# Kernel tuning notes

Hardware: AMD Instinct MI355X
Metric: run time of the kernel (lower is better)

Reference implementation:

```python
import jax, jax.numpy as jnp
import numpy as np

VOCAB, H, E_DIM, N_HEADS, MAXSEQ, L, N_ROUTED, TOPK = 32000, 1024, 512, 16, 1024, 4, 10, 3
EPS = 1e-5


def layernorm(x, g, b):
    m = jnp.mean(x, axis=-1, keepdims=True)
    v = jnp.mean((x - m) ** 2, axis=-1, keepdims=True)
    return (x - m) / jnp.sqrt(v + EPS) * g + b


def causal_attn(x, Wqkv, Wo):
    B, T, C = x.shape
    Dh = C // N_HEADS
    qkv = x @ Wqkv                                    # [B,T,3C]
    q, k, v = jnp.split(qkv, 3, axis=-1)
    def heads(t):  # [B,T,C] -> [B,Hh,T,Dh]
        return t.reshape(B, T, N_HEADS, Dh).transpose(0, 2, 1, 3)
    q, k, v = heads(q), heads(k), heads(v)
    scores = jnp.einsum('bhqd,bhkd->bhqk', q, k) / jnp.sqrt(jnp.float32(Dh))
    mask = jnp.tril(jnp.ones((T, T), dtype=bool))
    scores = jnp.where(mask, scores, jnp.finfo(scores.dtype).min)
    att = jax.nn.softmax(scores, axis=-1)
    y = jnp.einsum('bhqk,bhkd->bhqd', att, v)
    y = y.transpose(0, 2, 1, 3).reshape(B, T, C)
    return y @ Wo


def moe(x, Wr, Wsu, Wsd, Wu, Wd):
    # shared expert (n_shared=1)
    shared = jax.nn.gelu(x @ Wsu, approximate=False) @ Wsd
    # router + top-k gates
    probs = jax.nn.softmax(x @ Wr, axis=-1)           # [B,T,E]
    vals, idx = jax.lax.top_k(probs, TOPK)            # [B,T,k]
    gates = jnp.einsum('btke,btk->bte', jax.nn.one_hot(idx, N_ROUTED, dtype=x.dtype), vals)
    # routed experts: dense-over-experts compute, gate-weighted combine
    up = jax.nn.gelu(jnp.einsum('btd,edf->ebtf', x, Wu), approximate=False)
    out = jnp.einsum('ebtf,efd->ebtd', up, Wd)
    routed = jnp.einsum('ebtd,bte->btd', out, gates)
    return shared + routed


def forward(x, W_emb, W_pos, ln1_g, ln1_b, Wqkv, Wo, ln2_g, ln2_b,
            Wr, Wsu, Wsd, Wu, Wd, lnf_g, lnf_b):
    B, T = x.shape
    h = W_emb[x] + W_pos[:T][None, :, :]
    for l in range(L):
        a = causal_attn(layernorm(h, ln1_g[l], ln1_b[l]), Wqkv[l], Wo[l])
        a = a + h                                     # attn residual
        m = moe(layernorm(a, ln2_g[l], ln2_b[l]), Wr[l], Wsu[l], Wsd[l], Wu[l], Wd[l])
        h = m + h                                     # NOTE: residual from block INPUT (as in source)
    h = layernorm(h, lnf_g, lnf_b)
    logits = h[:, -1:, :] @ W_emb.T                   # tied head, last position only
    return logits


def setup_inputs() -> dict:
    key = jax.random.key(0)
    ks = jax.random.split(key, 16)
    s = 0.02
    d = {
        'x': jax.random.randint(ks[0], (4, 1024), 0, VOCAB),
        'W_emb': s * jax.random.normal(ks[1], (VOCAB, H), jnp.float32),
        'W_pos': s * jax.random.normal(ks[2], (MAXSEQ, H), jnp.float32),
        'ln1_g': jnp.ones((L, H), jnp.float32),
        'ln1_b': jnp.zeros((L, H), jnp.float32),
        'Wqkv': s * jax.random.normal(ks[3], (L, H, 3 * H), jnp.float32),
        'Wo': s * jax.random.normal(ks[4], (L, H, H), jnp.float32),
        'ln2_g': jnp.ones((L, H), jnp.float32),
        'ln2_b': jnp.zeros((L, H), jnp.float32),
        'Wr': s * jax.random.normal(ks[5], (L, H, N_ROUTED), jnp.float32),
        'Wsu': s * jax.random.normal(ks[6], (L, H, E_DIM), jnp.float32),
        'Wsd': s * jax.random.normal(ks[7], (L, E_DIM, H), jnp.float32),
        'Wu': s * jax.random.normal(ks[8], (L, N_ROUTED, H, E_DIM), jnp.float32),
        'Wd': s * jax.random.normal(ks[9], (L, N_ROUTED, E_DIM, H), jnp.float32),
        'lnf_g': jnp.ones((H,), jnp.float32),
        'lnf_b': jnp.zeros((H,), jnp.float32),
    }
    return d


def reference(x, W_emb, W_pos, ln1_g, ln1_b, Wqkv, Wo, ln2_g, ln2_b,
              Wr, Wsu, Wsd, Wu, Wd, lnf_g, lnf_b):
    return forward(x, W_emb, W_pos, ln1_g, ln1_b, Wqkv, Wo, ln2_g, ln2_b,
                   Wr, Wsu, Wsd, Wu, Wd, lnf_g, lnf_b)
```

## Files before the change

### kernel.cpp

```cpp
#include <hip/hip_runtime.h>
#include <hip/hip_bf16.h>
#include <math.h>

#define BT 4096
#define HD 1024
#define NHEAD 16
#define DH 64
#define ED 512
#define NEXP 10
#define NEXPA 11
#define TOPKE 3
#define NLAYER 4
#define NVOCAB 32000
#define NSLOT (BT * TOPKE)
#define NSLOTA (NSLOT + BT)
#define NSB 12

typedef __attribute__((ext_vector_type(8))) short bf16x8;
typedef __attribute__((ext_vector_type(4))) short bf16x4;
typedef __attribute__((ext_vector_type(4))) float f32x4;

__device__ __forceinline__ float gelu_f(float x) {
  return 0.5f * x * (1.0f + erff(x * 0.70710678118654752440f));
}

__device__ __forceinline__ void gll16(const void* g, void* l) {
  __builtin_amdgcn_global_load_lds(
      (const __attribute__((address_space(1))) unsigned int*)g,
      (__attribute__((address_space(3))) unsigned int*)l, 16, 0, 0);
}

__global__ __launch_bounds__(256) void k_embed_ln(const int* __restrict__ x,
                                                  const float* __restrict__ Wemb,
                                                  const float* __restrict__ Wpos,
                                                  const float* __restrict__ g,
                                                  const float* __restrict__ b,
                                                  float* __restrict__ h,
                                                  __hip_bfloat16* __restrict__ outb) {
  const int t = blockIdx.x;
  const int tid = threadIdx.x;
  const int pos = t & 1023;
  const int tok = x[t];
  float4 a = ((const float4*)(Wemb + (size_t)tok * HD))[tid];
  float4 p = ((const float4*)(Wpos + (size_t)pos * HD))[tid];
  float4 v = make_float4(a.x + p.x, a.y + p.y, a.z + p.z, a.w + p.w);
  ((float4*)(h + (size_t)t * HD))[tid] = v;
  float s = v.x + v.y + v.z + v.w;
  float ss = v.x * v.x + v.y * v.y + v.z * v.z + v.w * v.w;
#pragma unroll
  for (int o = 32; o > 0; o >>= 1) { s += __shfl_down(s, o); ss += __shfl_down(ss, o); }
  __shared__ float rs[4], rss[4];
  if ((tid & 63) == 0) { rs[tid >> 6] = s; rss[tid >> 6] = ss; }
  __syncthreads();
  const float S = rs[0] + rs[1] + rs[2] + rs[3];
  const float SS = rss[0] + rss[1] + rss[2] + rss[3];
  const float mean = S * (1.0f / HD);
  const float inv = rsqrtf(SS * (1.0f / HD) - mean * mean + 1e-5f);
  const float4 gg = ((const float4*)g)[tid];
  const float4 bb = ((const float4*)b)[tid];
  union { bf16x4 v; __hip_bfloat16 e[4]; } u;
  u.e[0] = __float2bfloat16((v.x - mean) * inv * gg.x + bb.x);
  u.e[1] = __float2bfloat16((v.y - mean) * inv * gg.y + bb.y);
  u.e[2] = __float2bfloat16((v.z - mean) * inv * gg.z + bb.z);
  u.e[3] = __float2bfloat16((v.w - mean) * inv * gg.w + bb.w);
  *(bf16x4*)(outb + (size_t)t * HD + tid * 4) = u.v;
}

__global__ __launch_bounds__(256) void k_wtrans(const float* __restrict__ in,
                                                __hip_bfloat16* __restrict__ out,
                                                int K, int N,
                                                int srcPer, int dstPer, int dstOff) {
  const int z = blockIdx.z;
  const int dz = (z / srcPer) * dstPer + (z % srcPer) + dstOff;
  const float* src = in + (size_t)z * K * N;
  __hip_bfloat16* dst = out + (size_t)dz * N * K;
  __shared__ float t[64][65];
  const int tid = threadIdx.x;
  const int k0 = blockIdx.y * 64, n0 = blockIdx.x * 64;
#pragma unroll
  for (int i = 0; i < 4; ++i) {
    const int r = (tid >> 4) + i * 16;
    const int c = (tid & 15) * 4;
    float4 v = *(const float4*)(src + (size_t)(k0 + r) * N + n0 + c);
    t[r][c] = v.x; t[r][c + 1] = v.y; t[r][c + 2] = v.z; t[r][c + 3] = v.w;
  }
  __syncthreads();
#pragma unroll
  for (int i = 0; i < 2; ++i) {
    const int n = (tid >> 3) + i * 32;
    const int k = (tid & 7) * 8;
    union { bf16x8 v; __hip_bfloat16 e[8]; } u;
#pragma unroll
    for (int j = 0; j < 8; ++j) u.e[j] = __float2bfloat16(t[k + j][n]);
    *(bf16x8*)(dst + (size_t)(n0 + n) * K + k0 + k) = u.v;
  }
}

__global__ __launch_bounds__(256) void k_wrtrans(const float* __restrict__ in,
                                                 float* __restrict__ out) {
  const int l = blockIdx.x;
  const float* src = in + (size_t)l * HD * NEXP;
  float* dst = out + (size_t)l * NEXP * HD;
  for (int idx = threadIdx.x; idx < NEXP * HD; idx += 256) {
    const int e = idx / HD, k = idx - e * HD;
    dst[idx] = src[(size_t)k * NEXP + e];
  }
}

__global__ __launch_bounds__(256) void k_vtrans(const __hip_bfloat16* __restrict__ qkv,
                                                __hip_bfloat16* __restrict__ vt) {
  const int bh = blockIdx.x, tt = blockIdx.y;
  const int b = bh >> 4, h = bh & 15;
  __shared__ __hip_bfloat16 t[64][72];
  for (int c = threadIdx.x; c < 512; c += 256) {
    int r = c >> 3, d0 = (c & 7) * 8;
    *(bf16x8*)&t[r][d0] =
        *(const bf16x8*)(qkv + ((size_t)(b * 1024 + tt * 64 + r)) * 3072 + 2048 + h * 64 + d0);
  }
  __syncthreads();
  for (int c = threadIdx.x; c < 512; c += 256) {
    int d = c >> 3, t0 = (c & 7) * 8;
    union { bf16x8 v; __hip_bfloat16 e[8]; } u;
#pragma unroll
    for (int j = 0; j < 8; ++j) u.e[j] = t[t0 + j][d];
    *(bf16x8*)(vt + ((size_t)(bh * 64 + d)) * 1024 + tt * 64 + t0) = u.v;
  }
}

__global__ __launch_bounds__(256) void k_ln_router(const __hip_bfloat16* __restrict__ in,
                                                   const float* __restrict__ g,
                                                   const float* __restrict__ b,
                                                   const float* __restrict__ Wrt,
                                                   __hip_bfloat16* __restrict__ outb,
                                                   float* __restrict__ gates,
                                                   int* __restrict__ eidx) {
  const int row = blockIdx.x;
  const int tid = threadIdx.x;
  __shared__ float xs[HD];
  __shared__ float rs[4], rss[4];
  __shared__ float lg[16];
  union { bf16x4 v; __hip_bfloat16 e[4]; } iv;
  iv.v = *(const bf16x4*)(in + (size_t)row * HD + tid * 4);
  const float4 v = make_float4(__bfloat162float(iv.e[0]), __bfloat162float(iv.e[1]),
                               __bfloat162float(iv.e[2]), __bfloat162float(iv.e[3]));
  float s = v.x + v.y + v.z + v.w;
  float ss = v.x * v.x + v.y * v.y + v.z * v.z + v.w * v.w;
#pragma unroll
  for (int o = 32; o > 0; o >>= 1) { s += __shfl_down(s, o); ss += __shfl_down(ss, o); }
  if ((tid & 63) == 0) { rs[tid >> 6] = s; rss[tid >> 6] = ss; }
  __syncthreads();
  const float S = rs[0] + rs[1] + rs[2] + rs[3];
  const float SS = rss[0] + rss[1] + rss[2] + rss[3];
  const float mean = S * (1.0f / HD);
  const float inv = rsqrtf(SS * (1.0f / HD) - mean * mean + 1e-5f);
  const float4 gg = ((const float4*)g)[tid];
  const float4 bb = ((const float4*)b)[tid];
  const float o0 = (v.x - mean) * inv * gg.x + bb.x;
  const float o1 = (v.y - mean) * inv * gg.y + bb.y;
  const float o2 = (v.z - mean) * inv * gg.z + bb.z;
  const float o3 = (v.w - mean) * inv * gg.w + bb.w;
  union { bf16x4 v; __hip_bfloat16 e[4]; } u;
  u.e[0] = __float2bfloat16(o0); u.e[1] = __float2bfloat16(o1);
  u.e[2] = __float2bfloat16(o2); u.e[3] = __float2bfloat16(o3);
  *(bf16x4*)(outb + (size_t)row * HD + tid * 4) = u.v;
  ((float4*)xs)[tid] = make_float4(o0, o1, o2, o3);
  __syncthreads();
  const int wv = tid >> 6, lane = tid & 63;
  for (int e = wv; e < NEXP; e += 4) {
    const float4* wr4 = (const float4*)(Wrt + (size_t)e * HD);
    float d = 0.f;
#pragma unroll
    for (int i = 0; i < 4; ++i) {
      float4 xv = ((const float4*)xs)[lane + i * 64];
      float4 wv4 = wr4[lane + i * 64];
      d += xv.x * wv4.x + xv.y * wv4.y + xv.z * wv4.z + xv.w * wv4.w;
    }
#pragma unroll
    for (int o = 32; o > 0; o >>= 1) d += __shfl_down(d, o);
    if (lane == 0) lg[e] = d;
  }
  __syncthreads();
  if (tid == 0) {
    float m = lg[0];
#pragma unroll
    for (int e = 1; e < NEXP; ++e) m = fmaxf(m, lg[e]);
    float p[NEXP], sum = 0.f;
#pragma unroll
    for (int e = 0; e < NEXP; ++e) { p[e] = __expf(lg[e] - m); sum += p[e]; }
    const float isum = 1.0f / sum;
#pragma unroll
    for (int e = 0; e < NEXP; ++e) p[e] *= isum;
    bool used[NEXP] = {};
    for (int k = 0; k < TOPKE; ++k) {
      int best = -1; float bv = -1.f;
      for (int e = 0; e < NEXP; ++e)
        if (!used[e] && p[e] > bv) { bv = p[e]; best = e; }
      used[best] = true;
      eidx[row * TOPKE + k] = best;
      gates[row * TOPKE + k] = bv;
    }
  }
}

__global__ __launch_bounds__(256) void k_lnf(const float* __restrict__ h,
                                             const float* __restrict__ g,
                                             const float* __restrict__ b,
                                             float* __restrict__ hf) {
  const int row = blockIdx.x * 1024 + 1023;
  const int tid = threadIdx.x;
  const float* xr = h + (size_t)row * HD;
  float s = 0.f, ss = 0.f;
  for (int i = tid; i < HD; i += 256) { float v = xr[i]; s += v; ss += v * v; }
#pragma unroll
  for (int o = 32; o > 0; o >>= 1) { s += __shfl_down(s, o); ss += __shfl_down(ss, o); }
  __shared__ float rs[4], rss[4];
  if ((tid & 63) == 0) { rs[tid >> 6] = s; rss[tid >> 6] = ss; }
  __syncthreads();
  const float S = rs[0] + rs[1] + rs[2] + rs[3];
  const float SS = rss[0] + rss[1] + rss[2] + rss[3];
  const float mean = S * (1.0f / HD);
  const float inv = rsqrtf(SS * (1.0f / HD) - mean * mean + 1e-5f);
  float* orow = hf + (size_t)blockIdx.x * HD;
  for (int i = tid; i < HD; i += 256) {
    float v = xr[i];
    orow[i] = (v - mean) * inv * g[i] + b[i];
  }
}

template <int EPI, int OBF>
__global__ __launch_bounds__(256) void k_mgemm(const __hip_bfloat16* __restrict__ A,
                                               const __hip_bfloat16* __restrict__ Bt,
                                               const float* __restrict__ R,
                                               float* __restrict__ C,
                                               __hip_bfloat16* __restrict__ Cb,
                                               int M, int N, int K) {
  __shared__ __hip_bfloat16 As[128 * 32];
  __shared__ __hip_bfloat16 Bs[128 * 32];
  const int tid = threadIdx.x;
  const int w = tid >> 6, lane = tid & 63;
  const int wr = w >> 1, wc = w & 1;
  const int m0 = blockIdx.y << 7, n0 = blockIdx.x << 7;
  const int srow = lane >> 2;
  const int scol = (lane & 3) * 8;
  const int kq = (lane >> 4) * 8;
  int aidx[4], bidx[4];
#pragma unroll
  for (int m = 0; m < 4; ++m) aidx[m] = (wr * 64 + m * 16 + (lane & 15)) * 32 + kq;
#pragma unroll
  for (int n = 0; n < 4; ++n) bidx[n] = (wc * 64 + n * 16 + (lane & 15)) * 32 + kq;

  f32x4 acc[4][4];
#pragma unroll
  for (int m = 0; m < 4; ++m)
#pragma unroll
    for (int n = 0; n < 4; ++n) acc[m][n] = (f32x4){0.f, 0.f, 0.f, 0.f};

  const __hip_bfloat16* ga = A + (size_t)(m0 + w * 32 + srow) * K + scol;
  const __hip_bfloat16* gb = Bt + (size_t)(n0 + w * 32 + srow) * K + scol;
  __hip_bfloat16* la0 = &As[(w * 32) * 32];
  __hip_bfloat16* la1 = &As[(w * 32 + 16) * 32];
  __hip_bfloat16* lb0 = &Bs[(w * 32) * 32];
  __hip_bfloat16* lb1 = &Bs[(w * 32 + 16) * 32];

  for (int k0 = 0; k0 < K; k0 += 32) {
    gll16(ga + k0, la0);
    gll16(ga + (size_t)16 * K + k0, la1);
    gll16(gb + k0, lb0);
    gll16(gb + (size_t)16 * K + k0, lb1);
    __syncthreads();
    bf16x8 af[4], bfv[4];
#pragma unroll
    for (int m = 0; m < 4; ++m) af[m] = *(const bf16x8*)&As[aidx[m]];
#pragma unroll
    for (int n = 0; n < 4; ++n) bfv[n] = *(const bf16x8*)&Bs[bidx[n]];
#pragma unroll
    for (int m = 0; m < 4; ++m)
#pragma unroll
      for (int n = 0; n < 4; ++n)
        acc[m][n] = __builtin_amdgcn_mfma_f32_16x16x32_bf16(af[m], bfv[n], acc[m][n], 0, 0, 0);
    __syncthreads();
  }

#pragma unroll
  for (int m = 0; m < 4; ++m) {
#pragma unroll
    for (int n = 0; n < 4; ++n) {
#pragma unroll
      for (int r = 0; r < 4; ++r) {
        const int row = m0 + wr * 64 + m * 16 + (lane >> 4) * 4 + r;
        const int col = n0 + wc * 64 + n * 16 + (lane & 15);
        float v = acc[m][n][r];
        if (EPI == 2) v += R[(size_t)row * N + col];
        if (OBF) Cb[(size_t)row * N + col] = __float2bfloat16(v);
        else C[(size_t)row * N + col] = v;
      }
    }
  }
}

template <int EPI>
__global__ __launch_bounds__(256) void k_mgemm_moe(const __hip_bfloat16* __restrict__ A,
                                                   const __hip_bfloat16* __restrict__ Btbase,
                                                   __hip_bfloat16* __restrict__ Cb,
                                                   const int* __restrict__ counts,
                                                   const int* __restrict__ offs,
                                                   const int* __restrict__ row_slot,
                                                   const float* __restrict__ gate_slot,
                                                   int N, int K, int gather) {
  int T = blockIdx.y;
  int e = -1, r0 = 0, acc0 = 0;
#pragma unroll
  for (int ee = 0; ee < NEXPA; ++ee) {
    const int nt = (counts[ee] + 127) >> 7;
    if (e < 0 && T < acc0 + nt) { e = ee; r0 = (T - acc0) << 7; }
    acc0 += nt;
  }
  if (e < 0) return;
  const int cnt = counts[e], off = offs[e];
  const __hip_bfloat16* Bt = Btbase + (size_t)e * N * K;

  __shared__ __hip_bfloat16 As[128 * 32];
  __shared__ __hip_bfloat16 Bs[128 * 32];
  const int tid = threadIdx.x;
  const int w = tid >> 6, lane = tid & 63;
  const int wr = w >> 1, wc = w & 1;
  const int n0 = blockIdx.x << 7;
  const int srow = lane >> 2;
  const int scol = (lane & 3) * 8;
  const int kq = (lane >> 4) * 8;
  int aidx[4], bidx[4];
#pragma unroll
  for (int m = 0; m < 4; ++m) aidx[m] = (wr * 64 + m * 16 + (lane & 15)) * 32 + kq;
#pragma unroll
  for (int n = 0; n < 4; ++n) bidx[n] = (wc * 64 + n * 16 + (lane & 15)) * 32 + kq;

  const int last = off + cnt - 1;
  int s0 = off + r0 + w * 32 + srow;        if (s0 > last) s0 = last;
  int s1 = off + r0 + w * 32 + 16 + srow;   if (s1 > last) s1 = last;
  const int arow0 = gather ? row_slot[s0] : s0;
  const int arow1 = gather ? row_slot[s1] : s1;

  f32x4 acc[4][4];
#pragma unroll
  for (int m = 0; m < 4; ++m)
#pragma unroll
    for (int n = 0; n < 4; ++n) acc[m][n] = (f32x4){0.f, 0.f, 0.f, 0.f};

  const __hip_bfloat16* ga0 = A + (size_t)arow0 * K + scol;
  const __hip_bfloat16* ga1 = A + (size_t)arow1 * K + scol;
  const __hip_bfloat16* gb = Bt + (size_t)(n0 + w * 32 + srow) * K + scol;
  __hip_bfloat16* la0 = &As[(w * 32) * 32];
  __hip_bfloat16* la1 = &As[(w * 32 + 16) * 32];
  __hip_bfloat16* lb0 = &Bs[(w * 32) * 32];
  __hip_bfloat16* lb1 = &Bs[(w * 32 + 16) * 32];

  for (int k0 = 0; k0 < K; k0 += 32) {
    gll16(ga0 + k0, la0);
    gll16(ga1 + k0, la1);
    gll16(gb + k0, lb0);
    gll16(gb + (size_t)16 * K + k0, lb1);
    __syncthreads();
    bf16x8 af[4], bfv[4];
#pragma unroll
    for (int m = 0; m < 4; ++m) af[m] = *(const bf16x8*)&As[aidx[m]];
#pragma unroll
    for (int n = 0; n < 4; ++n) bfv[n] = *(const bf16x8*)&Bs[bidx[n]];
#pragma unroll
    for (int m = 0; m < 4; ++m)
#pragma unroll
      for (int n = 0; n < 4; ++n)
        acc[m][n] = __builtin_amdgcn_mfma_f32_16x16x32_bf16(af[m], bfv[n], acc[m][n], 0, 0, 0);
    __syncthreads();
  }

#pragma unroll
  for (int m = 0; m < 4; ++m) {
#pragma unroll
    for (int r = 0; r < 4; ++r) {
      const int rl = wr * 64 + m * 16 + (lane >> 4) * 4 + r;
      if (r0 + rl < cnt) {
        const int slot = off + r0 + rl;
        const float sc = (EPI == 3) ? gate_slot[slot] : 1.0f;
#pragma unroll
        for (int n = 0; n < 4; ++n) {
          const int col = n0 + wc * 64 + n * 16 + (lane & 15);
          float v = acc[m][n][r];
          if (EPI == 1) v = gelu_f(v);
          else v *= sc;
          Cb[(size_t)slot * N + col] = __float2bfloat16(v);
        }
      }
    }
  }
}

__global__ __launch_bounds__(256) void k_mattn(const __hip_bfloat16* __restrict__ qkv,
                                               const __hip_bfloat16* __restrict__ vt,
                                               __hip_bfloat16* __restrict__ y) {
  const int bh = blockIdx.x;
  const int qt = 7 - (int)blockIdx.y;
  const int b = bh >> 4, hh = bh & 15;
  const int tid = threadIdx.x;
  const int w = tid >> 6, lane = tid & 63;
  const int l15 = lane & 15, g = lane >> 4;
  const int swl = (l15 & 7) << 3;

  __shared__ __hip_bfloat16 Ks[64 * 64];
  __shared__ __hip_bfloat16 Vs[64 * 64];
  __shared__ __hip_bfloat16 Pw[2][4][16 * 64];

  bf16x8 qf[2][2];
#pragma unroll
  for (int s = 0; s < 2; ++s) {
    const __hip_bfloat16* qp =
        qkv + ((size_t)(b * 1024 + qt * 128 + s * 64 + w * 16 + l15)) * 3072 + hh * 64 + g * 8;
    qf[s][0] = *(const bf16x8*)qp;
    qf[s][1] = *(const bf16x8*)(qp + 32);
  }

  f32x4 yacc[2][4];
#pragma unroll
  for (int s = 0; s < 2; ++s)
#pragma unroll
    for (int nt = 0; nt < 4; ++nt) yacc[s][nt] = (f32x4){0.f, 0.f, 0.f, 0.f};
  float m_s[2] = {-INFINITY, -INFINITY};
  float l_s[2] = {0.f, 0.f};
  const int qg0 = qt * 128 + w * 16 + l15;

  const int ktmax = 2 * qt + 1;
  for (int kt = 0; kt <= ktmax; ++kt) {
    __syncthreads();
#pragma unroll
    for (int c0 = 0; c0 < 512; c0 += 256) {
      const int c = c0 + tid;
      const int r = c >> 3, cc = (c & 7) * 8;
      const int sw = cc ^ ((r & 7) << 3);
      *(bf16x8*)&Ks[r * 64 + sw] =
          *(const bf16x8*)(qkv + ((size_t)(b * 1024 + kt * 64 + r)) * 3072 + 1024 + hh * 64 + cc);
      *(bf16x8*)&Vs[r * 64 + sw] =
          *(const bf16x8*)(vt + ((size_t)(bh * 64 + r)) * 1024 + kt * 64 + cc);
    }
    __syncthreads();
    bf16x8 kf[4][2];
#pragma unroll
    for (int m = 0; m < 4; ++m) {
      const int row = m * 16 + l15;
#pragma unroll
      for (int kk = 0; kk < 2; ++kk)
        kf[m][kk] = *(const bf16x8*)&Ks[row * 64 + ((kk * 32 + g * 8) ^ swl)];
    }
    bf16x8 pa[2][2] = {};
#pragma unroll
    for (int s = 0; s < 2; ++s) {
      if (kt > 2 * qt + s) continue;
      f32x4 st[4];
#pragma unroll
      for (int m = 0; m < 4; ++m) st[m] = (f32x4){0.f, 0.f, 0.f, 0.f};
#pragma unroll
      for (int m = 0; m < 4; ++m)
#pragma unroll
        for (int kk = 0; kk < 2; ++kk)
          st[m] = __builtin_amdgcn_mfma_f32_16x16x32_bf16(kf[m][kk], qf[s][kk], st[m], 0, 0, 0);
      const int qg = qg0 + s * 64;
      const bool dia = (kt == 2 * qt + s);
      float tmax = -INFINITY;
#pragma unroll
      for (int m = 0; m < 4; ++m)
#pragma unroll
        for (int r = 0; r < 4; ++r) {
          float v = st[m][r] * 0.125f;
          if (dia && (kt * 64 + m * 16 + g * 4 + r) > qg) v = -INFINITY;
          st[m][r] = v;
          tmax = fmaxf(tmax, v);
        }
      tmax = fmaxf(tmax, __shfl_xor(tmax, 16));
      tmax = fmaxf(tmax, __shfl_xor(tmax, 32));
      const float mnew = fmaxf(m_s[s], tmax);
      const float fac = __expf(m_s[s] - mnew);
      m_s[s] = mnew;
      float tsum = 0.f;
#pragma unroll
      for (int m = 0; m < 4; ++m)
#pragma unroll
        for (int r = 0; r < 4; ++r) {
          float p = __expf(st[m][r] - mnew);
          st[m][r] = p;
          tsum += p;
        }
      tsum += __shfl_xor(tsum, 16);
      tsum += __shfl_xor(tsum, 32);
      l_s[s] = l_s[s] * fac + tsum;
      float fq[4];
#pragma unroll
      for (int r = 0; r < 4; ++r) fq[r] = __shfl(fac, g * 4 + r);
#pragma unroll
      for (int nt = 0; nt < 4; ++nt)
#pragma unroll
        for (int r = 0; r < 4; ++r) yacc[s][nt][r] *= fq[r];
#pragma unroll
      for (int m = 0; m < 4; ++m) {
        union { bf16x4 v; __hip_bfloat16 e[4]; } pk;
#pragma unroll
        for (int r = 0; r < 4; ++r) pk.e[r] = __float2bfloat16(st[m][r]);
        *(bf16x4*)&Pw[s][w][l15 * 64 + ((m * 16 + g * 4) ^ swl)] = pk.v;
      }
#pragma unroll
      for (int kk = 0; kk < 2; ++kk)
        pa[s][kk] = *(const bf16x8*)&Pw[s][w][l15 * 64 + ((kk * 32 + g * 8) ^ swl)];
    }
    const bool v0 = (kt <= 2 * qt);
#pragma unroll
    for (int kk = 0; kk < 2; ++kk)
#pragma unroll
      for (int nt = 0; nt < 4; ++nt) {
        bf16x8 vf = *(const bf16x8*)&Vs[(nt * 16 + l15) * 64 + ((kk * 32 + g * 8) ^ swl)];
        if (v0) yacc[0][nt] = __builtin_amdgcn_mfma_f32_16x16x32_bf16(pa[0][kk], vf, yacc[0][nt], 0, 0, 0);
        yacc[1][nt] = __builtin_amdgcn_mfma_f32_16x16x32_bf16(pa[1][kk], vf, yacc[1][nt], 0, 0, 0);
      }
  }
#pragma unroll
  for (int s = 0; s < 2; ++s) {
    const float inv = 1.0f / l_s[s];
    float iq[4];
#pragma unroll
    for (int r = 0; r < 4; ++r) iq[r] = __shfl(inv, g * 4 + r);
#pragma unroll
    for (int r = 0; r < 4; ++r) {
      __hip_bfloat16* yp =
          y + ((size_t)(b * 1024 + qt * 128 + s * 64 + w * 16 + g * 4 + r)) * HD + hh * 64 + l15;
#pragma unroll
      for (int nt = 0; nt < 4; ++nt)
        yp[nt * 16] = __float2bfloat16(yacc[s][nt][r] * iq[r]);
    }
  }
}

__global__ __launch_bounds__(1024) void k_hist(const int* __restrict__ eidx,
                                               int* __restrict__ hist_g) {
  __shared__ int lh[16];
  const int tid = threadIdx.x;
  if (tid < 16) lh[tid] = 0;
  __syncthreads();
  atomicAdd(&lh[eidx[blockIdx.x * 1024 + tid]], 1);
  __syncthreads();
  if (tid < 16) hist_g[blockIdx.x * 16 + tid] = lh[tid];
}

__global__ __launch_bounds__(1024) void k_scatter2(const int* __restrict__ eidx,
                                                   const float* __restrict__ gates,
                                                   const int* __restrict__ hist_g,
                                                   int* __restrict__ counts,
                                                   int* __restrict__ offs,
                                                   int* __restrict__ row_slot,
                                                   float* __restrict__ gate_slot,
                                                   int* __restrict__ slot_of) {
  __shared__ int lcur[16];
  const int tid = threadIdx.x;
  const int blk = blockIdx.x;
  if (tid == 0) {
    int off = 0;
    for (int e = 0; e < NEXP; ++e) {
      int pre = 0, tot = 0;
      for (int b = 0; b < NSB; ++b) {
        const int hc = hist_g[b * 16 + e];
        if (b < blk) pre += hc;
        tot += hc;
      }
      lcur[e] = off + pre;
      if (blk == 0) { counts[e] = tot; offs[e] = off; }
      off += tot;
    }
    if (blk == 0) { counts[NEXP] = BT; offs[NEXP] = NSLOT; }
  }
  __syncthreads();
  const int i = blk * 1024 + tid;
  const int e = eidx[i];
  const int pos = atomicAdd(&lcur[e], 1);
  row_slot[pos] = i / TOPKE;
  gate_slot[pos] = gates[i];
  slot_of[i] = pos;
  if (i < BT) { row_slot[NSLOT + i] = i; gate_slot[NSLOT + i] = 1.0f; }
}

template <int DOLN>
__global__ __launch_bounds__(256) void k_combine_ln(float* __restrict__ h,
                                                    const __hip_bfloat16* __restrict__ rd,
                                                    const int* __restrict__ slot_of,
                                                    const float* __restrict__ g,
                                                    const float* __restrict__ b,
                                                    __hip_bfloat16* __restrict__ outb) {
  const int t = blockIdx.x;
  const int tid = threadIdx.x;
  const int s0 = slot_of[t * 3 + 0], s1 = slot_of[t * 3 + 1], s2 = slot_of[t * 3 + 2];
  const int s3 = NSLOT + t;
  float4 hv = ((float4*)(h + (size_t)t * HD))[tid];
  union { bf16x4 v; __hip_bfloat16 e[4]; } r0, r1, r2, r3;
  r0.v = *(const bf16x4*)(rd + (size_t)s0 * HD + tid * 4);
  r1.v = *(const bf16x4*)(rd + (size_t)s1 * HD + tid * 4);
  r2.v = *(const bf16x4*)(rd + (size_t)s2 * HD + tid * 4);
  r3.v = *(const bf16x4*)(rd + (size_t)s3 * HD + tid * 4);
  hv.x += __bfloat162float(r0.e[0]) + __bfloat162float(r1.e[0]) + __bfloat162float(r2.e[0]) + __bfloat162float(r3.e[0]);
  hv.y += __bfloat162float(r0.e[1]) + __bfloat162float(r1.e[1]) + __bfloat162float(r2.e[1]) + __bfloat162float(r3.e[1]);
  hv.z += __bfloat162float(r0.e[2]) + __bfloat162float(r1.e[2]) + __bfloat162float(r2.e[2]) + __bfloat162float(r3.e[2]);
  hv.w += __bfloat162float(r0.e[3]) + __bfloat162float(r1.e[3]) + __bfloat162float(r2.e[3]) + __bfloat162float(r3.e[3]);
  ((float4*)(h + (size_t)t * HD))[tid] = hv;
  if (DOLN) {
    float s = hv.x + hv.y + hv.z + hv.w;
    float ss = hv.x * hv.x + hv.y * hv.y + hv.z * hv.z + hv.w * hv.w;
#pragma unroll
    for (int o = 32; o > 0; o >>= 1) { s += __shfl_down(s, o); ss += __shfl_down(ss, o); }
    __shared__ float rs[4], rss[4];
    if ((tid & 63) == 0) { rs[tid >> 6] = s; rss[tid >> 6] = ss; }
    __syncthreads();
    const float S = rs[0] + rs[1] + rs[2] + rs[3];
    const float SS = rss[0] + rss[1] + rss[2] + rss[3];
    const float mean = S * (1.0f / HD);
    const float inv = rsqrtf(SS * (1.0f / HD) - mean * mean + 1e-5f);
    const float4 gg = ((const float4*)g)[tid];
    const float4 bb = ((const float4*)b)[tid];
    union { bf16x4 v; __hip_bfloat16 e[4]; } u;
    u.e[0] = __float2bfloat16((hv.x - mean) * inv * gg.x + bb.x);
    u.e[1] = __float2bfloat16((hv.y - mean) * inv * gg.y + bb.y);
    u.e[2] = __float2bfloat16((hv.z - mean) * inv * gg.z + bb.z);
    u.e[3] = __float2bfloat16((hv.w - mean) * inv * gg.w + bb.w);
    *(bf16x4*)(outb + (size_t)t * HD + tid * 4) = u.v;
  }
}

__global__ __launch_bounds__(256) void k_head(const float* __restrict__ hf,
                                              const float* __restrict__ Wemb,
                                              float* __restrict__ out) {
  __shared__ float hs[4][HD];
  const int tid = threadIdx.x;
  for (int i = tid; i < HD; i += 256) {
    hs[0][i] = hf[i]; hs[1][i] = hf[HD + i];
    hs[2][i] = hf[2 * HD + i]; hs[3][i] = hf[3 * HD + i];
  }
  __syncthreads();
  const int w = tid >> 6, lane = tid & 63;
  for (int i = 0; i < 4; ++i) {
    const int v = blockIdx.x * 16 + w * 4 + i;
    const float4* wr = (const float4*)(Wemb + (size_t)v * HD);
    float a0 = 0.f, a1 = 0.f, a2 = 0.f, a3 = 0.f;
    for (int q = lane; q < HD / 4; q += 64) {
      float4 wv = wr[q];
      const int k = q * 4;
      a0 += wv.x * hs[0][k] + wv.y * hs[0][k + 1] + wv.z * hs[0][k + 2] + wv.w * hs[0][k + 3];
      a1 += wv.x * hs[1][k] + wv.y * hs[1][k + 1] + wv.z * hs[1][k + 2] + wv.w * hs[1][k + 3];
      a2 += wv.x * hs[2][k] + wv.y * hs[2][k + 1] + wv.z * hs[2][k + 2] + wv.w * hs[2][k + 3];
      a3 += wv.x * hs[3][k] + wv.y * hs[3][k + 1] + wv.z * hs[3][k + 2] + wv.w * hs[3][k + 3];
    }
#pragma unroll
    for (int o = 32; o > 0; o >>= 1) {
      a0 += __shfl_down(a0, o); a1 += __shfl_down(a1, o);
      a2 += __shfl_down(a2, o); a3 += __shfl_down(a3, o);
    }
    if (lane == 0) {
      out[v] = a0; out[NVOCAB + v] = a1;
      out[2 * NVOCAB + v] = a2; out[3 * NVOCAB + v] = a3;
    }
  }
}

extern "C" void kernel_launch(void* const* d_in, const int* in_sizes, int n_in,
                              void* d_out, int out_size, void* d_ws, size_t ws_size,
                              hipStream_t stream) {
  (void)in_sizes; (void)n_in; (void)out_size; (void)ws_size;
  const int* x = (const int*)d_in[0];
  const float* W_emb = (const float*)d_in[1];
  const float* W_pos = (const float*)d_in[2];
  const float* ln1_g = (const float*)d_in[3];
  const float* ln1_b = (const float*)d_in[4];
  const float* Wqkv = (const float*)d_in[5];
  const float* Wo = (const float*)d_in[6];
  const float* ln2_g = (const float*)d_in[7];
  const float* ln2_b = (const float*)d_in[8];
  const float* Wr = (const float*)d_in[9];
  const float* Wsu = (const float*)d_in[10];
  const float* Wsd = (const float*)d_in[11];
  const float* Wu = (const float*)d_in[12];
  const float* Wd = (const float*)d_in[13];
  const float* lnf_g = (const float*)d_in[14];
  const float* lnf_b = (const float*)d_in[15];
  float* out = (float*)d_out;

  float* wsf = (float*)d_ws;
  size_t o = 0;
  float* hbuf = wsf + o; o += (size_t)BT * HD;
  float* hf = wsf + o; o += 4 * HD;
  float* gates = wsf + o; o += NSLOT;
  float* gate_slot = wsf + o; o += NSLOTA;
  int* eidx = (int*)(wsf + o); o += NSLOT;
  int* row_slot = (int*)(wsf + o); o += NSLOTA;
  int* slot_of = (int*)(wsf + o); o += NSLOT;
  int* counts = (int*)(wsf + o); o += 16;
  int* offs = (int*)(wsf + o); o += 16;
  int* hist_g = (int*)(wsf + o); o += NSB * 16;
  float* wr_t = wsf + o; o += (size_t)NLAYER * NEXP * HD;
  __hip_bfloat16* ab_bf  = (__hip_bfloat16*)(wsf + o); o += (size_t)BT * HD / 2;
  __hip_bfloat16* lno_bf = (__hip_bfloat16*)(wsf + o); o += (size_t)BT * HD / 2;
  __hip_bfloat16* ybf    = (__hip_bfloat16*)(wsf + o); o += (size_t)BT * HD / 2;
  __hip_bfloat16* rup_bf = (__hip_bfloat16*)(wsf + o); o += (size_t)NSLOTA * ED / 2;
  float* qkvreg = wsf + o; o += (size_t)BT * 3 * HD + (size_t)BT * HD / 2;
  __hip_bfloat16* wqkv_t = (__hip_bfloat16*)(wsf + o); o += (size_t)NLAYER * HD * 3 * HD / 2;
  __hip_bfloat16* wo_t   = (__hip_bfloat16*)(wsf + o); o += (size_t)NLAYER * HD * HD / 2;
  __hip_bfloat16* wu_t   = (__hip_bfloat16*)(wsf + o); o += (size_t)NLAYER * NEXPA * HD * ED / 2;
  __hip_bfloat16* wd_t   = (__hip_bfloat16*)(wsf + o); o += (size_t)NLAYER * NEXPA * ED * HD / 2;
  __hip_bfloat16* qkv_bf = (__hip_bfloat16*)qkvreg;
  __hip_bfloat16* vtb = qkv_bf + (size_t)BT * 3 * HD;
  __hip_bfloat16* rd_bf = (__hip_bfloat16*)qkvreg;

  k_wtrans<<<dim3(3 * HD / 64, HD / 64, NLAYER), 256, 0, stream>>>(
      Wqkv, wqkv_t, HD, 3 * HD, 1, 1, 0);
  k_wtrans<<<dim3(HD / 64, HD / 64, NLAYER), 256, 0, stream>>>(
      Wo, wo_t, HD, HD, 1, 1, 0);
  k_wtrans<<<dim3(ED / 64, HD / 64, NLAYER * NEXP), 256, 0, stream>>>(
      Wu, wu_t, HD, ED, NEXP, NEXPA, 0);
  k_wtrans<<<dim3(ED / 64, HD / 64, NLAYER), 256, 0, stream>>>(
      Wsu, wu_t, HD, ED, 1, NEXPA, NEXP);
  k_wtrans<<<dim3(HD / 64, ED / 64, NLAYER * NEXP), 256, 0, stream>>>(
      Wd, wd_t, ED, HD, NEXP, NEXPA, 0);
  k_wtrans<<<dim3(HD / 64, ED / 64, NLAYER), 256, 0, stream>>>(
      Wsd, wd_t, ED, HD, 1, NEXPA, NEXP);
  k_wrtrans<<<NLAYER, 256, 0, stream>>>(Wr, wr_t);

  k_embed_ln<<<BT, 256, 0, stream>>>(x, W_emb, W_pos, ln1_g, ln1_b, hbuf, lno_bf);

  for (int l = 0; l < NLAYER; ++l) {
    k_mgemm<0, 1><<<dim3(24, 32), 256, 0, stream>>>(
        lno_bf, wqkv_t + (size_t)l * HD * 3 * HD, nullptr, nullptr, qkv_bf, BT, 3 * HD, HD);
    k_vtrans<<<dim3(64, 16), 256, 0, stream>>>(qkv_bf, vtb);
    k_mattn<<<dim3(64, 8), 256, 0, stream>>>(qkv_bf, vtb, ybf);
    k_mgemm<2, 1><<<dim3(8, 32), 256, 0, stream>>>(
        ybf, wo_t + (size_t)l * HD * HD, hbuf, nullptr, ab_bf, BT, HD, HD);
    k_ln_router<<<BT, 256, 0, stream>>>(ab_bf, ln2_g + (size_t)l * HD, ln2_b + (size_t)l * HD,
                                        wr_t + (size_t)l * NEXP * HD, lno_bf, gates, eidx);
    k_hist<<<NSB, 1024, 0, stream>>>(eidx, hist_g);
    k_scatter2<<<NSB, 1024, 0, stream>>>(eidx, gates, hist_g, counts, offs,
                                         row_slot, gate_slot, slot_of);
    k_mgemm_moe<1><<<dim3(4, 160), 256, 0, stream>>>(
        lno_bf, wu_t + (size_t)l * NEXPA * HD * ED, rup_bf,
        counts, offs, row_slot, gate_slot, ED, HD, 1);
    k_mgemm_moe<3><<<dim3(8, 160), 256, 0, stream>>>(
        rup_bf, wd_t + (size_t)l * NEXPA * ED * HD, rd_bf,
        counts, offs, row_slot, gate_slot, HD, ED, 0);
    if (l < NLAYER - 1) {
      k_combine_ln<1><<<BT, 256, 0, stream>>>(hbuf, rd_bf, slot_of,
                                              ln1_g + (size_t)(l + 1) * HD,
                                              ln1_b + (size_t)(l + 1) * HD, lno_bf);
    } else {
      k_combine_ln<0><<<BT, 256, 0, stream>>>(hbuf, rd_bf, slot_of,
                                              nullptr, nullptr, nullptr);
    }
  }

  k_lnf<<<4, 256, 0, stream>>>(hbuf, lnf_g, lnf_b, hf);
  k_head<<<NVOCAB / 16, 256, 0, stream>>>(hf, W_emb, out);
}
```

Measured before the change: 1.102 ms.

## Double-buffer LDS tiles in dense and grouped MFMA GEMMs to overlap loads

Both the dense and the expert-grouped GEMM kernels now use two LDS buffers for the A and B tiles. Each iteration issues the global-to-LDS loads for the next K-slice before running MFMA on the current slice, so there is one barrier per slice instead of two and load latency can hide behind compute. This doubles LDS use per block, which may lower occupancy. It also relies on K being a multiple of 64 so the second compute step never reads an unfilled buffer; K is 512 or 1024 here, so that holds.

Result: faster. 1.027 ms (-6.8%).

```diff
diff --git a/kernel.cpp b/kernel.cpp
--- a/kernel.cpp
+++ b/kernel.cpp
@@ -227,6 +227,32 @@
   }
 }
 
+#define STAGE_AB(dA, dB, kk)                                  \
+  do {                                                        \
+    gll16(ga + (kk), &dA[(w * 32) * 32]);                     \
+    gll16(ga + (size_t)16 * K + (kk), &dA[(w * 32 + 16) * 32]); \
+    gll16(gb + (kk), &dB[(w * 32) * 32]);                     \
+    gll16(gb + (size_t)16 * K + (kk), &dB[(w * 32 + 16) * 32]); \
+  } while (0)
+
+#define STAGE_AB2(dA, dB, kk)                                 \
+  do {                                                        \
+    gll16(ga0 + (kk), &dA[(w * 32) * 32]);                    \
+    gll16(ga1 + (kk), &dA[(w * 32 + 16) * 32]);               \
+    gll16(gb + (kk), &dB[(w * 32) * 32]);                     \
+    gll16(gb + (size_t)16 * K + (kk), &dB[(w * 32 + 16) * 32]); \
+  } while (0)
+
+#define COMPUTE_AB(sA, sB)                                                        \
+  do {                                                                            \
+    bf16x8 af[4], bfv[4];                                                         \
+    _Pragma("unroll") for (int m = 0; m < 4; ++m) af[m] = *(const bf16x8*)&sA[aidx[m]]; \
+    _Pragma("unroll") for (int n = 0; n < 4; ++n) bfv[n] = *(const bf16x8*)&sB[bidx[n]]; \
+    _Pragma("unroll") for (int m = 0; m < 4; ++m)                                 \
+      _Pragma("unroll") for (int n = 0; n < 4; ++n)                               \
+        acc[m][n] = __builtin_amdgcn_mfma_f32_16x16x32_bf16(af[m], bfv[n], acc[m][n], 0, 0, 0); \
+  } while (0)
+
 template <int EPI, int OBF>
 __global__ __launch_bounds__(256) void k_mgemm(const __hip_bfloat16* __restrict__ A,
                                                const __hip_bfloat16* __restrict__ Bt,
@@ -234,8 +260,10 @@
                                                float* __restrict__ C,
                                                __hip_bfloat16* __restrict__ Cb,
                                                int M, int N, int K) {
-  __shared__ __hip_bfloat16 As[128 * 32];
-  __shared__ __hip_bfloat16 Bs[128 * 32];
+  __shared__ __hip_bfloat16 As0[128 * 32];
+  __shared__ __hip_bfloat16 Bs0[128 * 32];
+  __shared__ __hip_bfloat16 As1[128 * 32];
+  __shared__ __hip_bfloat16 Bs1[128 * 32];
   const int tid = threadIdx.x;
   const int w = tid >> 6, lane = tid & 63;
   const int wr = w >> 1, wc = w & 1;
@@ -257,27 +285,15 @@
 
   const __hip_bfloat16* ga = A + (size_t)(m0 + w * 32 + srow) * K + scol;
   const __hip_bfloat16* gb = Bt + (size_t)(n0 + w * 32 + srow) * K + scol;
-  __hip_bfloat16* la0 = &As[(w * 32) * 32];
-  __hip_bfloat16* la1 = &As[(w * 32 + 16) * 32];
-  __hip_bfloat16* lb0 = &Bs[(w * 32) * 32];
-  __hip_bfloat16* lb1 = &Bs[(w * 32 + 16) * 32];
-
-  for (int k0 = 0; k0 < K; k0 += 32) {
-    gll16(ga + k0, la0);
-    gll16(ga + (size_t)16 * K + k0, la1);
-    gll16(gb + k0, lb0);
-    gll16(gb + (size_t)16 * K + k0, lb1);
+
+  STAGE_AB(As0, Bs0, 0);
+  __syncthreads();
+  for (int k0 = 0; k0 < K; k0 += 64) {
+    if (k0 + 32 < K) STAGE_AB(As1, Bs1, k0 + 32);
+    COMPUTE_AB(As0, Bs0);
     __syncthreads();
-    bf16x8 af[4], bfv[4];
-#pragma unroll
-    for (int m = 0; m < 4; ++m) af[m] = *(const bf16x8*)&As[aidx[m]];
-#pragma unroll
-    for (int n = 0; n < 4; ++n) bfv[n] = *(const bf16x8*)&Bs[bidx[n]];
-#pragma unroll
-    for (int m = 0; m < 4; ++m)
-#pragma unroll
-      for (int n = 0; n < 4; ++n)
-        acc[m][n] = __builtin_amdgcn_mfma_f32_16x16x32_bf16(af[m], bfv[n], acc[m][n], 0, 0, 0);
+    if (k0 + 64 < K) STAGE_AB(As0, Bs0, k0 + 64);
+    COMPUTE_AB(As1, Bs1);
     __syncthreads();
   }
 
@@ -319,8 +335,10 @@
   const int cnt = counts[e], off = offs[e];
   const __hip_bfloat16* Bt = Btbase + (size_t)e * N * K;
 
-  __shared__ __hip_bfloat16 As[128 * 32];
-  __shared__ __hip_bfloat16 Bs[128 * 32];
+  __shared__ __hip_bfloat16 As0[128 * 32];
+  __shared__ __hip_bfloat16 Bs0[128 * 32];
+  __shared__ __hip_bfloat16 As1[128 * 32];
+  __shared__ __hip_bfloat16 Bs1[128 * 32];
   const int tid = threadIdx.x;
   const int w = tid >> 6, lane = tid & 63;
   const int wr = w >> 1, wc = w & 1;
@@ -349,27 +367,15 @@
   const __hip_bfloat16* ga0 = A + (size_t)arow0 * K + scol;
   const __hip_bfloat16* ga1 = A + (size_t)arow1 * K + scol;
   const __hip_bfloat16* gb = Bt + (size_t)(n0 + w * 32 + srow) * K + scol;
-  __hip_bfloat16* la0 = &As[(w * 32) * 32];
-  __hip_bfloat16* la1 = &As[(w * 32 + 16) * 32];
-  __hip_bfloat16* lb0 = &Bs[(w * 32) * 32];
-  __hip_bfloat16* lb1 = &Bs[(w * 32 + 16) * 32];
-
-  for (int k0 = 0; k0 < K; k0 += 32) {
-    gll16(ga0 + k0, la0);
-    gll16(ga1 + k0, la1);
-    gll16(gb + k0, lb0);
-    gll16(gb + (size_t)16 * K + k0, lb1);
+
+  STAGE_AB2(As0, Bs0, 0);
+  __syncthreads();
+  for (int k0 = 0; k0 < K; k0 += 64) {
+    if (k0 + 32 < K) STAGE_AB2(As1, Bs1, k0 + 32);
+    COMPUTE_AB(As0, Bs0);
     __syncthreads();
-    bf16x8 af[4], bfv[4];
-#pragma unroll
-    for (int m = 0; m < 4; ++m) af[m] = *(const bf16x8*)&As[aidx[m]];
-#pragma unroll
-    for (int n = 0; n < 4; ++n) bfv[n] = *(const bf16x8*)&Bs[bidx[n]];
-#pragma unroll
-    for (int m = 0; m < 4; ++m)
-#pragma unroll
-      for (int n = 0; n < 4; ++n)
-        acc[m][n] = __builtin_amdgcn_mfma_f32_16x16x32_bf16(af[m], bfv[n], acc[m][n], 0, 0, 0);
+    if (k0 + 64 < K) STAGE_AB2(As0, Bs0, k0 + 64);
+    COMPUTE_AB(As1, Bs1);
     __syncthreads();
   }
 
```
